# Kernel tuning notes

Measured on AMD Instinct MI355X. Metric: run time of the kernel, lower is better.

Reference implementation:

```python
import jax, jax.numpy as jnp
import numpy as np

BN_EPS = 1e-5
NORM_EPS = 1e-6


def _nearest_resize(m, H, W):
    # torch F.interpolate(mode='nearest'): idx = floor(i * in/out)
    B, C, h, w = m.shape
    iy = (jnp.arange(H) * h) // H
    ix = (jnp.arange(W) * w) // W
    return m[:, :, iy][:, :, :, ix]


def _distance_transform(m_s):
    # Euclidean distance of every pixel to nearest foreground pixel (mask>0.5),
    # normalized per-sample to [0,1]; all-background samples -> ones map.
    B, _, H, W = m_s.shape
    HW = H * W
    yy, xx = jnp.meshgrid(jnp.arange(H, dtype=jnp.float32),
                          jnp.arange(W, dtype=jnp.float32), indexing='ij')
    ys, xs = yy.reshape(-1), xx.reshape(-1)
    # shared [HW, HW] pairwise squared distances (same for all batch elems)
    D2 = (ys[:, None] - ys[None, :]) ** 2 + (xs[:, None] - xs[None, :]) ** 2
    fg = m_s.reshape(B, HW) > 0.5                                  # [B, HW]
    min_d2 = jnp.min(jnp.where(fg[:, None, :], D2[None], jnp.inf), axis=-1)  # [B, HW]
    has_fg = fg.any(axis=1, keepdims=True)
    dist = jnp.where(has_fg, jnp.sqrt(min_d2), 1.0)
    mx = dist.max(axis=1, keepdims=True)
    dist = dist / (mx + NORM_EPS)
    return dist.reshape(B, 1, H, W)


def _forward(f_s, supp_feat_bin, support_mask, w_fusion, gamma, beta):
    B, C, H, W = f_s.shape
    m_s = _nearest_resize(support_mask, H, W)
    attn = jax.nn.sigmoid(jnp.sum(f_s * supp_feat_bin, axis=1, keepdims=True))  # [B,1,H,W]
    f_w = f_s * attn
    dist = _distance_transform(m_s)
    fusion_in = jnp.concatenate([f_s, supp_feat_bin, f_w, dist], axis=1)  # [B,3C+1,H,W]
    y = jnp.einsum('oc,bchw->bohw', w_fusion, fusion_in)  # 1x1 conv, no bias
    # BatchNorm2d in training mode: biased batch stats over (B,H,W)
    mean = y.mean(axis=(0, 2, 3))
    var = y.var(axis=(0, 2, 3))
    yn = (y - mean[None, :, None, None]) * jax.lax.rsqrt(var[None, :, None, None] + BN_EPS)
    return jax.nn.relu(yn * gamma[None, :, None, None] + beta[None, :, None, None])


def setup_inputs() -> dict:
    key = jax.random.key(0)
    k1, k2, k3, k4 = jax.random.split(key, 4)
    B, C, H, W = 8, 256, 64, 64
    Hm, Wm = 256, 256
    return {
        'f_s': jax.random.normal(k1, (B, C, H, W), dtype=jnp.float32),
        'supp_feat_bin': jax.random.normal(k2, (B, C, H, W), dtype=jnp.float32),
        'support_mask': jax.random.uniform(k3, (B, 1, Hm, Wm), dtype=jnp.float32),
        'w_fusion': jax.random.normal(k4, (C, 3 * C + 1), dtype=jnp.float32) * 0.02,
        'gamma': jnp.ones((C,), dtype=jnp.float32),
        'beta': jnp.zeros((C,), dtype=jnp.float32),
    }


def reference(f_s, supp_feat_bin, support_mask, w_fusion, gamma, beta):
    return _forward(f_s, supp_feat_bin, support_mask, w_fusion, gamma, beta)
```

## Files before the change

kernel.cpp:

```cpp
#include <hip/hip_runtime.h>
#include <math.h>

#define C_IN   256
#define HW_    4096
#define KW_    769
#define NPIX_BN 32768.0f

typedef short bf16x8 __attribute__((ext_vector_type(8)));
typedef float f32x4  __attribute__((ext_vector_type(4)));
typedef unsigned short u16x8 __attribute__((ext_vector_type(8)));

__device__ inline unsigned short f2bf(float x){
    unsigned u = __float_as_uint(x);
    u += 0x7fffu + ((u >> 16) & 1u);
    return (unsigned short)(u >> 16);
}
__device__ inline float bf2f(unsigned short h){
    return __uint_as_float(((unsigned)h) << 16);
}

#define GLOAD16(gp, lp) \
    __builtin_amdgcn_global_load_lds( \
        (const __attribute__((address_space(1))) void*)(gp), \
        (__attribute__((address_space(3))) void*)(lp), 16, 0, 0)

__global__ __launch_bounds__(256) void prep_w(
    const float* __restrict__ w, unsigned short* __restrict__ wp)
{
    int idx = blockIdx.x * 256 + threadIdx.x;
    int j  = idx & 7;
    int o  = (idx >> 3) & 255;
    int t2 = idx >> 11;
    int c  = (t2 >> 2) * 32 + (t2 & 3) * 8 + j;
    wp[idx] = f2bf(w[(size_t)o * KW_ + c]);
}

__global__ __launch_bounds__(256) void conv_kernel(
    const float* __restrict__ f_s, const float* __restrict__ sfb,
    unsigned short* __restrict__ xf, unsigned short* __restrict__ xs,
    unsigned short* __restrict__ xw)
{
    __shared__ float red[4][64];
    __shared__ float attn_sm[64];
    int blk = blockIdx.x;
    int t = threadIdx.x, lane = t & 63, g = t >> 6;
    int b = blk >> 6;
    int p = (blk & 63) * 64 + lane;
    const float* fB = f_s + (size_t)b * C_IN * HW_ + p;
    const float* sB = sfb + (size_t)b * C_IN * HW_ + p;
    u16x8* XF = (u16x8*)xf;
    u16x8* XS = (u16x8*)xs;
    u16x8* XW = (u16x8*)xw;

    float ap = 0.f;
    u16x8 xfreg[8];
    float fv[8], sv[8], fv2[8], sv2[8];
    #pragma unroll
    for (int j = 0; j < 8; ++j) {
        fv[j] = fB[(size_t)(g * 8 + j) * HW_];
        sv[j] = sB[(size_t)(g * 8 + j) * HW_];
    }
    #pragma unroll
    for (int ks = 0; ks < 8; ++ks) {
        if (ks < 7) {
            #pragma unroll
            for (int j = 0; j < 8; ++j) {
                fv2[j] = fB[(size_t)((ks + 1) * 32 + g * 8 + j) * HW_];
                sv2[j] = sB[(size_t)((ks + 1) * 32 + g * 8 + j) * HW_];
            }
        }
        u16x8 pf, ps;
        #pragma unroll
        for (int j = 0; j < 8; ++j) {
            ap += fv[j] * sv[j];
            pf[j] = f2bf(fv[j]);
            ps[j] = f2bf(sv[j]);
        }
        int plane = (b * 8 + ks) * 4 + g;
        XF[(size_t)plane * HW_ + p] = pf;
        XS[(size_t)plane * HW_ + p] = ps;
        xfreg[ks] = pf;
        #pragma unroll
        for (int j = 0; j < 8; ++j) { fv[j] = fv2[j]; sv[j] = sv2[j]; }
    }
    red[g][lane] = ap;
    __syncthreads();
    if (t < 64) {
        float a = red[0][t] + red[1][t] + red[2][t] + red[3][t];
        attn_sm[t] = 1.f / (1.f + __expf(-a));
    }
    __syncthreads();
    float at = attn_sm[lane];
    #pragma unroll
    for (int ks = 0; ks < 8; ++ks) {
        u16x8 pw;
        #pragma unroll
        for (int j = 0; j < 8; ++j)
            pw[j] = f2bf(bf2f(xfreg[ks][j]) * at);
        XW[(size_t)((b * 8 + ks) * 4 + g) * HW_ + p] = pw;
    }
}

__global__ __launch_bounds__(512) void dist_kernel(
    const float* __restrict__ mask, float* __restrict__ dist_raw,
    unsigned* __restrict__ dmax)
{
    __shared__ unsigned fg[4096];
    __shared__ int cnt;
    __shared__ float wmax[8];
    int b = blockIdx.x, tile = blockIdx.y;
    int t = threadIdx.x, lane = t & 63;
    if (t == 0) cnt = 0;
    __syncthreads();
    const float* mb = mask + (size_t)b * 65536;
    #pragma unroll
    for (int r = 0; r < 8; ++r) {
        int pp = r * 512 + t;
        int i = pp >> 6, j = pp & 63;
        bool pred = mb[i * 1024 + j * 4] > 0.5f;
        unsigned long long bal = __ballot(pred);
        int base = 0;
        if (lane == 0) base = atomicAdd(&cnt, __popcll(bal));
        base = __shfl(base, 0, 64);
        if (pred)
            fg[base + __popcll(bal & ((1ull << lane) - 1ull))] =
                (unsigned)((i << 8) | j);
    }
    __syncthreads();
    int nfg = cnt;
    int pix = tile * 128 + (t >> 2);
    int q = t & 3;
    int py = pix >> 6, px = pix & 63;
    int md = 0x7fffffff;
    #pragma unroll 4
    for (int it = q; it < nfg; it += 4) {
        unsigned e = fg[it];
        int dy = py - (int)(e >> 8);
        int dx = px - (int)(e & 255u);
        int d2 = dy * dy + dx * dx;
        md = min(md, d2);
    }
    md = min(md, __shfl_xor(md, 1, 64));
    md = min(md, __shfl_xor(md, 2, 64));
    float d = (nfg == 0) ? 1.0f : sqrtf((float)md);
    if (q == 0) dist_raw[b * HW_ + pix] = d;
    float mm = d;
    #pragma unroll
    for (int off = 1; off < 64; off <<= 1)
        mm = fmaxf(mm, __shfl_xor(mm, off, 64));
    if (lane == 0) wmax[t >> 6] = mm;
    __syncthreads();
    if (t == 0) {
        float M = wmax[0];
        #pragma unroll
        for (int i = 1; i < 8; ++i) M = fmaxf(M, wmax[i]);
        atomicMax(dmax + b, __float_as_uint(M));
    }
}

__global__ __launch_bounds__(256) void gemm_kernel(
    const unsigned short* __restrict__ xf, const unsigned short* __restrict__ xs,
    const unsigned short* __restrict__ xw, const unsigned short* __restrict__ wprep,
    const float* __restrict__ w,
    const float* __restrict__ dist_raw, const unsigned* __restrict__ dmax,
    unsigned short* __restrict__ ybf,
    float* __restrict__ gsum, float* __restrict__ gsumsq)
{
    __shared__ u16x8 LA[512];
    __shared__ u16x8 LX[512];

    int bx = blockIdx.x;
    int ot = bx & 1, nt = bx >> 1;
    int oBase = ot * 128, nBase = nt * 128;
    int b = nBase >> 12, pBase = nBase & 4095;
    int t = threadIdx.x, lane = t & 63, g = t >> 6;
    int wo = g >> 1, wn = g & 1;
    int l15 = lane & 15, kq = lane >> 4;
    int oW = oBase + wo * 64;

    const u16x8* WPc = (const u16x8*)wprep;
    const u16x8* XFc = (const u16x8*)xf;
    const u16x8* XSc = (const u16x8*)xs;
    const u16x8* XWc = (const u16x8*)xw;
    const bf16x8* LAr = (const bf16x8*)LA;
    const bf16x8* LXr = (const bf16x8*)LX;

    int kq0 = t >> 7;
    int kq1 = 2 + (t >> 7);
    int rl  = t & 127;
    u16x8* dstA0 = &LA[g * 64];
    u16x8* dstA1 = &LA[256 + g * 64];
    u16x8* dstX0 = &LX[g * 64];
    u16x8* dstX1 = &LX[256 + g * 64];

    f32x4 acc[4][4];
    #pragma unroll
    for (int fo = 0; fo < 4; ++fo)
        #pragma unroll
        for (int fn = 0; fn < 4; ++fn)
            acc[fo][fn] = (f32x4){0.f, 0.f, 0.f, 0.f};

    #pragma unroll
    for (int kn = 0; kn < 24; ++kn) {
        int k8 = kn & 7;
        const u16x8* Xsel = (kn < 8) ? XFc : ((kn < 16) ? XSc : XWc);
        GLOAD16(WPc + (kn * 4 + kq0) * 256 + oBase + rl, dstA0);
        GLOAD16(WPc + (kn * 4 + kq1) * 256 + oBase + rl, dstA1);
        GLOAD16(Xsel + (size_t)((b * 8 + k8) * 4 + kq0) * HW_ + pBase + rl, dstX0);
        GLOAD16(Xsel + (size_t)((b * 8 + k8) * 4 + kq1) * HW_ + pBase + rl, dstX1);
        __syncthreads();
        bf16x8 af[4], xr[4];
        #pragma unroll
        for (int fo = 0; fo < 4; ++fo)
            af[fo] = LAr[kq * 128 + wo * 64 + fo * 16 + l15];
        #pragma unroll
        for (int fn = 0; fn < 4; ++fn)
            xr[fn] = LXr[kq * 128 + wn * 64 + fn * 16 + l15];
        #pragma unroll
        for (int fo = 0; fo < 4; ++fo)
            #pragma unroll
            for (int fn = 0; fn < 4; ++fn)
                acc[fo][fn] = __builtin_amdgcn_mfma_f32_16x16x32_bf16(
                    af[fo], xr[fn], acc[fo][fn], 0, 0, 0);
        __syncthreads();
    }

    float dinv = 1.0f / (__uint_as_float(dmax[b]) + 1e-6f);
    const float* dR = dist_raw + b * HW_ + pBase + wn * 64;
    float dn[4];
    #pragma unroll
    for (int fn = 0; fn < 4; ++fn)
        dn[fn] = dR[fn * 16 + l15] * dinv;

    float s_acc[4][4], ss_acc[4][4];
    #pragma unroll
    for (int fo = 0; fo < 4; ++fo) {
        #pragma unroll
        for (int r = 0; r < 4; ++r) {
            int o = oW + fo * 16 + kq * 4 + r;
            float wd = w[(size_t)o * KW_ + 768];
            float s = 0.f, ss = 0.f;
            #pragma unroll
            for (int fn = 0; fn < 4; ++fn) {
                float v = acc[fo][fn][r] + wd * dn[fn];
                ybf[((size_t)(b * C_IN + o)) * HW_ + pBase + wn * 64 + fn * 16 + l15] = f2bf(v);
                s += v; ss += v * v;
            }
            s_acc[fo][r] = s; ss_acc[fo][r] = ss;
        }
    }
    #pragma unroll
    for (int m = 8; m; m >>= 1) {
        #pragma unroll
        for (int fo = 0; fo < 4; ++fo)
            #pragma unroll
            for (int r = 0; r < 4; ++r) {
                s_acc[fo][r]  += __shfl_xor(s_acc[fo][r],  m, 64);
                ss_acc[fo][r] += __shfl_xor(ss_acc[fo][r], m, 64);
            }
    }
    if (l15 == 0) {
        #pragma unroll
        for (int fo = 0; fo < 4; ++fo)
            #pragma unroll
            for (int r = 0; r < 4; ++r) {
                int o = oW + fo * 16 + kq * 4 + r;
                atomicAdd(&gsum[o],   s_acc[fo][r]);
                atomicAdd(&gsumsq[o], ss_acc[fo][r]);
            }
    }
}

__global__ __launch_bounds__(256) void bn_kernel(
    const float* __restrict__ gsum, const float* __restrict__ gsumsq,
    const float* __restrict__ gamma, const float* __restrict__ beta,
    const unsigned short* __restrict__ ybf, float* __restrict__ out)
{
    int bo = blockIdx.x;
    int o = bo & 255;
    float mean = gsum[o] * (1.0f / NPIX_BN);
    float var  = gsumsq[o] * (1.0f / NPIX_BN) - mean * mean;
    float sc = gamma[o] * rsqrtf(var + 1e-5f);
    float sh = beta[o] - mean * sc;
    const u16x8* yp = (const u16x8*)(ybf + (size_t)bo * HW_);
    float4* op = (float4*)(out + (size_t)bo * HW_);
    int t = threadIdx.x;
    #pragma unroll
    for (int r = 0; r < 2; ++r) {
        u16x8 v = yp[r * 256 + t];
        float4 lo, hi;
        lo.x = fmaxf(bf2f(v[0]) * sc + sh, 0.f);
        lo.y = fmaxf(bf2f(v[1]) * sc + sh, 0.f);
        lo.z = fmaxf(bf2f(v[2]) * sc + sh, 0.f);
        lo.w = fmaxf(bf2f(v[3]) * sc + sh, 0.f);
        hi.x = fmaxf(bf2f(v[4]) * sc + sh, 0.f);
        hi.y = fmaxf(bf2f(v[5]) * sc + sh, 0.f);
        hi.z = fmaxf(bf2f(v[6]) * sc + sh, 0.f);
        hi.w = fmaxf(bf2f(v[7]) * sc + sh, 0.f);
        op[(r * 256 + t) * 2]     = lo;
        op[(r * 256 + t) * 2 + 1] = hi;
    }
}

extern "C" void kernel_launch(void* const* d_in, const int* in_sizes, int n_in,
                              void* d_out, int out_size, void* d_ws, size_t ws_size,
                              hipStream_t stream)
{
    const float* f_s   = (const float*)d_in[0];
    const float* sfb   = (const float*)d_in[1];
    const float* mask  = (const float*)d_in[2];
    const float* w     = (const float*)d_in[3];
    const float* gamma = (const float*)d_in[4];
    const float* beta  = (const float*)d_in[5];
    float* out = (float*)d_out;
    float* ws  = (float*)d_ws;

    float*          dist_raw = ws;
    unsigned*       dmax     = (unsigned*)(ws + 32768);
    float*          gsum     = ws + 32784;
    float*          gsumsq   = ws + 33040;
    unsigned short* wprep    = (unsigned short*)(ws + 33296);

    const size_t P1_need = ((size_t)131600 + 4 * 4194304) * 4;
    unsigned short *xf, *xs, *xw, *ybf;
    if (ws_size >= P1_need) {
        xf  = (unsigned short*)(ws + 131600);
        xs  = (unsigned short*)(ws + 131600 + 1 * (size_t)4194304);
        xw  = (unsigned short*)(ws + 131600 + 2 * (size_t)4194304);
        ybf = (unsigned short*)(ws + 131600 + 3 * (size_t)4194304);
    } else {
        xf  = (unsigned short*)d_out;
        xs  = ((unsigned short*)d_out) + 8388608;
        xw  = (unsigned short*)(ws + 131600);
        ybf = (unsigned short*)(ws + 131600 + (size_t)4194304);
    }

    hipMemsetAsync(ws + 32768, 0, (33296 - 32768) * 4, stream);

    prep_w<<<768, 256, 0, stream>>>(w, wprep);
    conv_kernel<<<512, 256, 0, stream>>>(f_s, sfb, xf, xs, xw);
    dist_kernel<<<dim3(8, 32), 512, 0, stream>>>(mask, dist_raw, dmax);
    gemm_kernel<<<512, 256, 0, stream>>>(xf, xs, xw, wprep, w, dist_raw,
                                         dmax, ybf, gsum, gsumsq);
    bn_kernel<<<2048, 256, 0, stream>>>(gsum, gsumsq, gamma, beta, ybf, out);
}
```

Measured before the change: 229.2 us.

## Double-buffer GEMM LDS staging, remap blocks, and widen conv kernel to 512 threads

The GEMM kernel now keeps two LDS buffers and issues the async global-to-LDS loads for the next K-step before computing on the current one, so load latency can overlap the MFMA work. Block indices are permuted so neighbouring blocks fall on different groups, which may change how L2/MALL is shared across XCDs. The conv/prep kernel doubles its threads per block, splitting the channel loop across 8 waves so each thread does half the iterations. The cost is twice the LDS per GEMM block, which can lower occupancy, and a larger reduction in the conv kernel.

```diff
diff --git a/kernel.cpp b/kernel.cpp
--- a/kernel.cpp
+++ b/kernel.cpp
@@ -35,17 +35,19 @@
     wp[idx] = f2bf(w[(size_t)o * KW_ + c]);
 }
 
-__global__ __launch_bounds__(256) void conv_kernel(
+__global__ __launch_bounds__(512) void conv_kernel(
     const float* __restrict__ f_s, const float* __restrict__ sfb,
     unsigned short* __restrict__ xf, unsigned short* __restrict__ xs,
     unsigned short* __restrict__ xw)
 {
-    __shared__ float red[4][64];
+    __shared__ float red[8][64];
     __shared__ float attn_sm[64];
     int blk = blockIdx.x;
     int t = threadIdx.x, lane = t & 63, g = t >> 6;
     int b = blk >> 6;
     int p = (blk & 63) * 64 + lane;
+    int kq  = g & 3;
+    int ks0 = g >> 2;
     const float* fB = f_s + (size_t)b * C_IN * HW_ + p;
     const float* sB = sfb + (size_t)b * C_IN * HW_ + p;
     u16x8* XF = (u16x8*)xf;
@@ -53,20 +55,23 @@
     u16x8* XW = (u16x8*)xw;
 
     float ap = 0.f;
-    u16x8 xfreg[8];
+    u16x8 xfreg[4];
     float fv[8], sv[8], fv2[8], sv2[8];
     #pragma unroll
     for (int j = 0; j < 8; ++j) {
-        fv[j] = fB[(size_t)(g * 8 + j) * HW_];
-        sv[j] = sB[(size_t)(g * 8 + j) * HW_];
-    }
-    #pragma unroll
-    for (int ks = 0; ks < 8; ++ks) {
-        if (ks < 7) {
+        int c = ks0 * 32 + kq * 8 + j;
+        fv[j] = fB[(size_t)c * HW_];
+        sv[j] = sB[(size_t)c * HW_];
+    }
+    #pragma unroll
+    for (int i = 0; i < 4; ++i) {
+        int ks = ks0 + 2 * i;
+        if (i < 3) {
             #pragma unroll
             for (int j = 0; j < 8; ++j) {
-                fv2[j] = fB[(size_t)((ks + 1) * 32 + g * 8 + j) * HW_];
-                sv2[j] = sB[(size_t)((ks + 1) * 32 + g * 8 + j) * HW_];
+                int c = (ks + 2) * 32 + kq * 8 + j;
+                fv2[j] = fB[(size_t)c * HW_];
+                sv2[j] = sB[(size_t)c * HW_];
             }
         }
         u16x8 pf, ps;
@@ -76,28 +81,29 @@
             pf[j] = f2bf(fv[j]);
             ps[j] = f2bf(sv[j]);
         }
-        int plane = (b * 8 + ks) * 4 + g;
+        int plane = (b * 8 + ks) * 4 + kq;
         XF[(size_t)plane * HW_ + p] = pf;
         XS[(size_t)plane * HW_ + p] = ps;
-        xfreg[ks] = pf;
+        xfreg[i] = pf;
         #pragma unroll
         for (int j = 0; j < 8; ++j) { fv[j] = fv2[j]; sv[j] = sv2[j]; }
     }
     red[g][lane] = ap;
     __syncthreads();
     if (t < 64) {
-        float a = red[0][t] + red[1][t] + red[2][t] + red[3][t];
+        float a = red[0][t] + red[1][t] + red[2][t] + red[3][t]
+                + red[4][t] + red[5][t] + red[6][t] + red[7][t];
         attn_sm[t] = 1.f / (1.f + __expf(-a));
     }
     __syncthreads();
     float at = attn_sm[lane];
     #pragma unroll
-    for (int ks = 0; ks < 8; ++ks) {
+    for (int i = 0; i < 4; ++i) {
         u16x8 pw;
         #pragma unroll
         for (int j = 0; j < 8; ++j)
-            pw[j] = f2bf(bf2f(xfreg[ks][j]) * at);
-        XW[(size_t)((b * 8 + ks) * 4 + g) * HW_ + p] = pw;
+            pw[j] = f2bf(bf2f(xfreg[i][j]) * at);
+        XW[(size_t)((b * 8 + ks0 + 2 * i) * 4 + kq) * HW_ + p] = pw;
     }
 }
 
@@ -166,11 +172,12 @@
     unsigned short* __restrict__ ybf,
     float* __restrict__ gsum, float* __restrict__ gsumsq)
 {
-    __shared__ u16x8 LA[512];
-    __shared__ u16x8 LX[512];
-
-    int bx = blockIdx.x;
-    int ot = bx & 1, nt = bx >> 1;
+    __shared__ u16x8 LA[2][512];
+    __shared__ u16x8 LX[2][512];
+
+    int bx0 = blockIdx.x;
+    int v = (bx0 & 7) * 64 + (bx0 >> 3);
+    int ot = v & 1, nt = v >> 1;
     int oBase = ot * 128, nBase = nt * 128;
     int b = nBase >> 12, pBase = nBase & 4095;
     int t = threadIdx.x, lane = t & 63, g = t >> 6;
@@ -182,16 +189,18 @@
     const u16x8* XFc = (const u16x8*)xf;
     const u16x8* XSc = (const u16x8*)xs;
     const u16x8* XWc = (const u16x8*)xw;
-    const bf16x8* LAr = (const bf16x8*)LA;
-    const bf16x8* LXr = (const bf16x8*)LX;
 
     int kq0 = t >> 7;
     int kq1 = 2 + (t >> 7);
     int rl  = t & 127;
-    u16x8* dstA0 = &LA[g * 64];
-    u16x8* dstA1 = &LA[256 + g * 64];
-    u16x8* dstX0 = &LX[g * 64];
-    u16x8* dstX1 = &LX[256 + g * 64];
+
+#define STAGE(buf, kn) { \
+    int _k8 = (kn) & 7; \
+    const u16x8* _Xs = ((kn) < 8) ? XFc : (((kn) < 16) ? XSc : XWc); \
+    GLOAD16(WPc + ((kn) * 4 + kq0) * 256 + oBase + rl, &LA[buf][g * 64]); \
+    GLOAD16(WPc + ((kn) * 4 + kq1) * 256 + oBase + rl, &LA[buf][256 + g * 64]); \
+    GLOAD16(_Xs + (size_t)((b * 8 + _k8) * 4 + kq0) * HW_ + pBase + rl, &LX[buf][g * 64]); \
+    GLOAD16(_Xs + (size_t)((b * 8 + _k8) * 4 + kq1) * HW_ + pBase + rl, &LX[buf][256 + g * 64]); }
 
     f32x4 acc[4][4];
     #pragma unroll
@@ -200,15 +209,15 @@
         for (int fn = 0; fn < 4; ++fn)
             acc[fo][fn] = (f32x4){0.f, 0.f, 0.f, 0.f};
 
+    STAGE(0, 0);
+    __syncthreads();
+
     #pragma unroll
     for (int kn = 0; kn < 24; ++kn) {
-        int k8 = kn & 7;
-        const u16x8* Xsel = (kn < 8) ? XFc : ((kn < 16) ? XSc : XWc);
-        GLOAD16(WPc + (kn * 4 + kq0) * 256 + oBase + rl, dstA0);
-        GLOAD16(WPc + (kn * 4 + kq1) * 256 + oBase + rl, dstA1);
-        GLOAD16(Xsel + (size_t)((b * 8 + k8) * 4 + kq0) * HW_ + pBase + rl, dstX0);
-        GLOAD16(Xsel + (size_t)((b * 8 + k8) * 4 + kq1) * HW_ + pBase + rl, dstX1);
-        __syncthreads();
+        int cur = kn & 1;
+        if (kn < 23) STAGE(cur ^ 1, kn + 1);
+        const bf16x8* LAr = (const bf16x8*)&LA[cur][0];
+        const bf16x8* LXr = (const bf16x8*)&LX[cur][0];
         bf16x8 af[4], xr[4];
         #pragma unroll
         for (int fo = 0; fo < 4; ++fo)
@@ -224,6 +233,7 @@
                     af[fo], xr[fn], acc[fo][fn], 0, 0, 0);
         __syncthreads();
     }
+#undef STAGE
 
     float dinv = 1.0f / (__uint_as_float(dmax[b]) + 1e-6f);
     const float* dR = dist_raw + b * HW_ + pBase + wn * 64;
@@ -242,9 +252,9 @@
             float s = 0.f, ss = 0.f;
             #pragma unroll
             for (int fn = 0; fn < 4; ++fn) {
-                float v = acc[fo][fn][r] + wd * dn[fn];
-                ybf[((size_t)(b * C_IN + o)) * HW_ + pBase + wn * 64 + fn * 16 + l15] = f2bf(v);
-                s += v; ss += v * v;
+                float vv = acc[fo][fn][r] + wd * dn[fn];
+                ybf[((size_t)(b * C_IN + o)) * HW_ + pBase + wn * 64 + fn * 16 + l15] = f2bf(vv);
+                s += vv; ss += vv * vv;
             }
             s_acc[fo][r] = s; ss_acc[fo][r] = ss;
         }
@@ -338,7 +348,7 @@
     hipMemsetAsync(ws + 32768, 0, (33296 - 32768) * 4, stream);
 
     prep_w<<<768, 256, 0, stream>>>(w, wprep);
-    conv_kernel<<<512, 256, 0, stream>>>(f_s, sfb, xf, xs, xw);
+    conv_kernel<<<512, 512, 0, stream>>>(f_s, sfb, xf, xs, xw);
     dist_kernel<<<dim3(8, 32), 512, 0, stream>>>(mask, dist_raw, dmax);
     gemm_kernel<<<512, 256, 0, stream>>>(xf, xs, xw, wprep, w, dist_raw,
                                          dmax, ybf, gsum, gsumsq);
```

New measurement: 227.8 us. Within noise of the previous version (-0.6%).
